# Optimization experiments

Measured on AMD Instinct MI355X. Metric: run time of the kernel, lower is better.

Reference implementation:

```python
import jax, jax.numpy as jnp
import numpy as np

N = 30000      # nodes
E = 300000     # directed edges (self loops added in conv)
G = 128        # graphs in the batch
IN = 128       # input_dim
HID = 64       # hidden per head
HEADS = 4
NC = 10        # num_classes
EPS = 1e-5
SLOPE = 0.2    # GATv2 leaky_relu negative slope


def setup_inputs() -> dict:
    key = jax.random.key(0)
    ks = jax.random.split(key, 40)
    d = {}
    d['x'] = jax.random.normal(ks[0], (N, IN), jnp.float32)
    d['edge_index'] = jax.random.randint(ks[1], (2, E), 0, N, jnp.int32)
    d['batch'] = jnp.sort(jax.random.randint(ks[2], (N,), 0, G, jnp.int32))
    in_ch = [IN, HID * HEADS, HID * HEADS, HID * HEADS]
    for i in range(4):
        oc = HID * HEADS if i < 3 else HID  # last layer concat=False -> HID
        sc = 1.0 / np.sqrt(in_ch[i])
        d[f'Wl{i}'] = jax.random.normal(ks[3 + 6 * i], (in_ch[i], HID * HEADS), jnp.float32) * sc
        d[f'Wr{i}'] = jax.random.normal(ks[4 + 6 * i], (in_ch[i], HID * HEADS), jnp.float32) * sc
        d[f'att{i}'] = jax.random.normal(ks[5 + 6 * i], (HEADS, HID), jnp.float32) * 0.1
        d[f'b{i}'] = jnp.zeros((oc,), jnp.float32)
        d[f'bng{i}'] = jnp.ones((oc,), jnp.float32)
        d[f'bnb{i}'] = jnp.zeros((oc,), jnp.float32)
    d['fc1_w'] = jax.random.normal(ks[30], (HID, HID), jnp.float32) / np.sqrt(HID)
    d['fc1_b'] = jnp.zeros((HID,), jnp.float32)
    d['fc2_w'] = jax.random.normal(ks[31], (HID, NC), jnp.float32) / np.sqrt(HID)
    d['fc2_b'] = jnp.zeros((NC,), jnp.float32)
    return d


def _gatv2_conv(h, src, dst, Wl, Wr, att, b, concat):
    # GATv2Conv: x_l = lin_l(x) for sources, x_r = lin_r(x) for targets
    xl = (h @ Wl).reshape(N, HEADS, HID)
    xr = (h @ Wr).reshape(N, HEADS, HID)
    z = jax.nn.leaky_relu(xl[src] + xr[dst], SLOPE)       # [Et, H, C]
    e = jnp.einsum('ehc,hc->eh', z, att)                   # [Et, H]
    m = jax.ops.segment_max(e, dst, num_segments=N)        # per-dst max
    p = jnp.exp(e - m[dst])
    s = jax.ops.segment_sum(p, dst, num_segments=N)
    alpha = p / s[dst]                                     # segment softmax
    msg = alpha[..., None] * xl[src]                       # [Et, H, C]
    out = jax.ops.segment_sum(msg, dst, num_segments=N)    # [N, H, C]
    out = out.reshape(N, HEADS * HID) if concat else out.mean(axis=1)
    return out + b


def _bn_train(h, g, b):
    mu = h.mean(axis=0)
    var = h.var(axis=0)  # biased, as torch BN uses for normalization
    return g * (h - mu) * jax.lax.rsqrt(var + EPS) + b


def _forward(x, edge_index, batch,
             Wl0, Wr0, att0, b0, bng0, bnb0,
             Wl1, Wr1, att1, b1, bng1, bnb1,
             Wl2, Wr2, att2, b2, bng2, bnb2,
             Wl3, Wr3, att3, b3, bng3, bnb3,
             fc1_w, fc1_b, fc2_w, fc2_b):
    loops = jnp.arange(N, dtype=edge_index.dtype)
    src = jnp.concatenate([edge_index[0], loops])  # add_self_loops=True
    dst = jnp.concatenate([edge_index[1], loops])
    layers = [(Wl0, Wr0, att0, b0, bng0, bnb0, True),
              (Wl1, Wr1, att1, b1, bng1, bnb1, True),
              (Wl2, Wr2, att2, b2, bng2, bnb2, True),
              (Wl3, Wr3, att3, b3, bng3, bnb3, False)]
    h = x
    for Wl, Wr, att, b, g, bb, concat in layers:
        h = jax.nn.elu(_bn_train(_gatv2_conv(h, src, dst, Wl, Wr, att, b, concat), g, bb))
    sums = jax.ops.segment_sum(h, batch, num_segments=G)
    cnt = jax.ops.segment_sum(jnp.ones((N,), h.dtype), batch, num_segments=G)
    pooled = sums / jnp.maximum(cnt, 1.0)[:, None]         # global_mean_pool
    o = jax.nn.relu(pooled @ fc1_w + fc1_b)
    return o @ fc2_w + fc2_b                               # dropout off (eval)


def reference(x, edge_index, batch,
              Wl0, Wr0, att0, b0, bng0, bnb0,
              Wl1, Wr1, att1, b1, bng1, bnb1,
              Wl2, Wr2, att2, b2, bng2, bnb2,
              Wl3, Wr3, att3, b3, bng3, bnb3,
              fc1_w, fc1_b, fc2_w, fc2_b):
    return _forward(x, edge_index, batch,
                    Wl0, Wr0, att0, b0, bng0, bnb0,
                    Wl1, Wr1, att1, b1, bng1, bnb1,
                    Wl2, Wr2, att2, b2, bng2, bnb2,
                    Wl3, Wr3, att3, b3, bng3, bnb3,
                    fc1_w, fc1_b, fc2_w, fc2_b)
```

## Files before the change

### kernel.cpp

```cpp
#include <hip/hip_runtime.h>
#include <hip/hip_bf16.h>
#include <math.h>

#define NN    30000
#define MPAD  30080
#define EE    300000
#define ETOT  330000
#define GG    128
#define IND   128
#define HIDD  64
#define NHEAD 4
#define CC    256
#define NCL   10
#define EPSBN 1e-5f
#define SLOPE 0.2f

typedef __attribute__((ext_vector_type(8))) __bf16 bf16x8;
typedef __attribute__((ext_vector_type(4))) float f32x4;

__device__ inline float b2f(unsigned u16) {
    union { unsigned i; float f; } c; c.i = u16 << 16; return c.f;
}
__device__ inline unsigned short f2b(float f) {
    __hip_bfloat16 b = __float2bfloat16(f);
    unsigned short u; __builtin_memcpy(&u, &b, 2); return u;
}
__device__ inline void unpack8(uint4 u, float* f) {
    f[0] = b2f(u.x & 0xffffu); f[1] = b2f(u.x >> 16);
    f[2] = b2f(u.y & 0xffffu); f[3] = b2f(u.y >> 16);
    f[4] = b2f(u.z & 0xffffu); f[5] = b2f(u.z >> 16);
    f[6] = b2f(u.w & 0xffffu); f[7] = b2f(u.w >> 16);
}

__global__ void k_deg(const int* __restrict__ ei, int* __restrict__ deg) {
    int e = blockIdx.x * blockDim.x + threadIdx.x;
    if (e >= ETOT) return;
    int d = (e < EE) ? ei[EE + e] : (e - EE);
    atomicAdd(&deg[d], 1);
}

__global__ void k_scan(const int* __restrict__ deg, int* __restrict__ rowptr,
                       int* __restrict__ cursor) {
    const int PER = 30;
    int t = threadIdx.x;
    int base = t * PER;
    int loc[PER];
    int s = 0;
    #pragma unroll
    for (int j = 0; j < PER; ++j) {
        int v = (base + j < NN) ? deg[base + j] : 0;
        loc[j] = s; s += v;
    }
    int lane = t & 63, wid = t >> 6;
    int v = s;
    #pragma unroll
    for (int d = 1; d < 64; d <<= 1) {
        int u = __shfl_up(v, d, 64);
        if (lane >= d) v += u;
    }
    __shared__ int wsum[16], woff[16];
    if (lane == 63) wsum[wid] = v;
    __syncthreads();
    if (t == 0) { int a = 0; for (int w2 = 0; w2 < 16; ++w2) { woff[w2] = a; a += wsum[w2]; } }
    __syncthreads();
    int excl = woff[wid] + (v - s);
    #pragma unroll
    for (int j = 0; j < PER; ++j) {
        int idx = base + j;
        if (idx <= NN) { int val = excl + loc[j]; rowptr[idx] = val; cursor[idx] = val; }
    }
}

__global__ void k_scatter(const int* __restrict__ ei, int* __restrict__ cursor,
                          int* __restrict__ csrc) {
    int e = blockIdx.x * blockDim.x + threadIdx.x;
    if (e >= ETOT) return;
    int s, d;
    if (e < EE) { s = ei[e]; d = ei[EE + e]; } else { s = e - EE; d = s; }
    int pos = atomicAdd(&cursor[d], 1);
    csrc[pos] = s;
}

struct WPtrs { const float* wl[4]; const float* wr[4]; };

__global__ void k_prep(WPtrs p, const float* __restrict__ x,
                       __hip_bfloat16* __restrict__ wt, __hip_bfloat16* __restrict__ hb) {
    int id = blockIdx.x * 256 + threadIdx.x;
    if (id < 65536) {
        int n = id >> 7, k = id & 127;
        float v = (n < 256) ? p.wl[0][(size_t)k * 256 + n] : p.wr[0][(size_t)k * 256 + n - 256];
        wt[id] = __float2bfloat16(v);
    } else if (id < 458752) {
        int id2 = id - 65536;
        int li = 1 + (id2 >> 17);
        int r = id2 & 131071;
        int n = r >> 8, k = r & 255;
        float v = (n < 256) ? p.wl[li][(size_t)k * 256 + n] : p.wr[li][(size_t)k * 256 + n - 256];
        wt[id] = __float2bfloat16(v);
    } else {
        int id2 = id - 458752;
        if (id2 < NN * IND) hb[id2] = __float2bfloat16(x[id2]);
    }
}

template<int K>
__global__ __launch_bounds__(256) void k_gemm_mfma(
        const __hip_bfloat16* __restrict__ A, const __hip_bfloat16* __restrict__ Wt,
        __hip_bfloat16* __restrict__ xlb, __hip_bfloat16* __restrict__ xrb) {
    __shared__ __bf16 As[128 * 40];
    __shared__ __bf16 Bs[128 * 40];
    const int t = threadIdx.x;
    const int row0 = blockIdx.x * 128;
    const int col0 = blockIdx.y * 128;
    const int wv = t >> 6, lane = t & 63;
    const int wm = (wv & 1) * 64, wn = (wv >> 1) * 64;
    const int lm = lane & 15, lq = lane >> 4;
    const int sr0 = t >> 2, scc = (t & 3) * 8;
    const int sr1 = sr0 + 64;
    uint4 va0, va1, vb0, vb1;
    va0 = *(const uint4*)&A [(size_t)(row0 + sr0) * K + scc];
    va1 = *(const uint4*)&A [(size_t)(row0 + sr1) * K + scc];
    vb0 = *(const uint4*)&Wt[(size_t)(col0 + sr0) * K + scc];
    vb1 = *(const uint4*)&Wt[(size_t)(col0 + sr1) * K + scc];
    f32x4 acc[4][4] = {};
    for (int k0 = 0; k0 < K; k0 += 32) {
        *(uint4*)&As[sr0 * 40 + scc] = va0;
        *(uint4*)&As[sr1 * 40 + scc] = va1;
        *(uint4*)&Bs[sr0 * 40 + scc] = vb0;
        *(uint4*)&Bs[sr1 * 40 + scc] = vb1;
        __syncthreads();
        if (k0 + 32 < K) {
            int kn = k0 + 32;
            va0 = *(const uint4*)&A [(size_t)(row0 + sr0) * K + kn + scc];
            va1 = *(const uint4*)&A [(size_t)(row0 + sr1) * K + kn + scc];
            vb0 = *(const uint4*)&Wt[(size_t)(col0 + sr0) * K + kn + scc];
            vb1 = *(const uint4*)&Wt[(size_t)(col0 + sr1) * K + kn + scc];
        }
        bf16x8 af[4], bfr[4];
        #pragma unroll
        for (int i = 0; i < 4; ++i) {
            af[i]  = *(bf16x8*)&As[(wm + i * 16 + lm) * 40 + lq * 8];
            bfr[i] = *(bf16x8*)&Bs[(wn + i * 16 + lm) * 40 + lq * 8];
        }
        #pragma unroll
        for (int i = 0; i < 4; ++i)
            #pragma unroll
            for (int j = 0; j < 4; ++j)
                acc[i][j] = __builtin_amdgcn_mfma_f32_16x16x32_bf16(af[i], bfr[j], acc[i][j], 0, 0, 0);
        __syncthreads();
    }
    const int crow = lq * 4;
    __hip_bfloat16* O = (blockIdx.y < 2) ? xlb : xrb;
    const int cbase = (blockIdx.y & 1) * 128 + wn;
    #pragma unroll
    for (int j = 0; j < 4; ++j) {
        int oc = cbase + j * 16 + lm;
        #pragma unroll
        for (int i = 0; i < 4; ++i) {
            int grow = row0 + wm + i * 16 + crow;
            #pragma unroll
            for (int r = 0; r < 4; ++r)
                O[(size_t)(grow + r) * CC + oc] = __float2bfloat16(acc[i][j][r]);
        }
    }
}

template<bool CONCAT>
__global__ __launch_bounds__(256) void k_gat(const __hip_bfloat16* __restrict__ xlb,
        const __hip_bfloat16* __restrict__ xrb, const int* __restrict__ rowptr,
        const int* __restrict__ csrc, const float* __restrict__ att,
        __hip_bfloat16* __restrict__ outb, float* __restrict__ outf) {
    const int wv = threadIdx.x >> 6, lane = threadIdx.x & 63;
    const int n = blockIdx.x * 4 + wv;
    if (n >= NN) return;
    const int sub = lane >> 5, l5 = lane & 31;
    const float4* att4 = (const float4*)att;
    float4 a0 = att4[l5 * 2], a1 = att4[l5 * 2 + 1];
    float aw[8] = {a0.x, a0.y, a0.z, a0.w, a1.x, a1.y, a1.z, a1.w};
    const uint4* xl4 = (const uint4*)xlb;
    const uint4* xr4 = (const uint4*)xrb;
    float xrv[8]; unpack8(xr4[(size_t)n * 32 + l5], xrv);
    const int beg = rowptr[n], end = rowptr[n + 1];
    float ssum = 0.f;
    float acc[8] = {};
    for (int i0 = beg; i0 < end; i0 += 2) {
        int i = i0 + sub;
        bool valid = i < end;
        int s = csrc[valid ? i : end - 1];
        float xlv[8]; unpack8(xl4[(size_t)s * 32 + l5], xlv);
        float tv = 0.f;
        #pragma unroll
        for (int j = 0; j < 8; ++j) {
            float v = xlv[j] + xrv[j];
            v = fmaxf(v, SLOPE * v);
            tv = fmaf(v, aw[j], tv);
        }
        tv += __shfl_xor(tv, 1);
        tv += __shfl_xor(tv, 2);
        tv += __shfl_xor(tv, 4);
        float p = valid ? __expf(tv) : 0.f;
        ssum += p;
        #pragma unroll
        for (int j = 0; j < 8; ++j) acc[j] = fmaf(p, xlv[j], acc[j]);
    }
    ssum += __shfl_xor(ssum, 32);
    #pragma unroll
    for (int j = 0; j < 8; ++j) acc[j] += __shfl_xor(acc[j], 32);
    float inv = 1.f / ssum;
    if (CONCAT) {
        if (sub == 0) {
            unsigned short r[8];
            #pragma unroll
            for (int j = 0; j < 8; ++j) r[j] = f2b(acc[j] * inv);
            uint4 o;
            o.x = r[0] | ((unsigned)r[1] << 16); o.y = r[2] | ((unsigned)r[3] << 16);
            o.z = r[4] | ((unsigned)r[5] << 16); o.w = r[6] | ((unsigned)r[7] << 16);
            ((uint4*)outb)[(size_t)n * 32 + l5] = o;
        }
    } else {
        float v[8];
        #pragma unroll
        for (int j = 0; j < 8; ++j) {
            v[j] = acc[j] * inv;
            v[j] += __shfl_xor(v[j], 8);
            v[j] += __shfl_xor(v[j], 16);
            v[j] *= 0.25f;
        }
        if (lane < 8) {
            ((float4*)outf)[(size_t)n * 16 + lane * 2]     = make_float4(v[0], v[1], v[2], v[3]);
            ((float4*)outf)[(size_t)n * 16 + lane * 2 + 1] = make_float4(v[4], v[5], v[6], v[7]);
        }
    }
}

__global__ __launch_bounds__(256) void k_bnstats256b(const __hip_bfloat16* __restrict__ in,
                                                     float* __restrict__ stats) {
    __shared__ float sh[512];
    int r0 = blockIdx.x * 128;
    int rend = min(r0 + 128, NN);
    int t = threadIdx.x;
    int half = t >> 7, tc = t & 127;
    float s0 = 0.f, s1 = 0.f, q0 = 0.f, q1 = 0.f;
    const unsigned* u32 = (const unsigned*)in;
    for (int r = r0 + half; r < rend; r += 2) {
        unsigned w = u32[(size_t)r * 128 + tc];
        float a = b2f(w & 0xffffu), b = b2f(w >> 16);
        s0 += a; q0 += a * a; s1 += b; q1 += b * b;
    }
    if (half) {
        sh[tc * 4 + 0] = s0; sh[tc * 4 + 1] = s1;
        sh[tc * 4 + 2] = q0; sh[tc * 4 + 3] = q1;
    }
    __syncthreads();
    if (!half) {
        s0 += sh[tc * 4 + 0]; s1 += sh[tc * 4 + 1];
        q0 += sh[tc * 4 + 2]; q1 += sh[tc * 4 + 3];
        atomicAdd(&stats[2 * tc], s0);       atomicAdd(&stats[2 * tc + 1], s1);
        atomicAdd(&stats[256 + 2 * tc], q0); atomicAdd(&stats[256 + 2 * tc + 1], q1);
    }
}

__global__ __launch_bounds__(256) void k_bnelu256b(const __hip_bfloat16* __restrict__ in,
        const float* __restrict__ stats, const float* __restrict__ gamma,
        const float* __restrict__ beta, __hip_bfloat16* __restrict__ outb) {
    int id = blockIdx.x * 256 + threadIdx.x;
    if (id >= NN * 32) return;
    int c0 = (id & 31) * 8;
    uint4 u = ((const uint4*)in)[id];
    float f[8]; unpack8(u, f);
    unsigned short r[8];
    #pragma unroll
    for (int j = 0; j < 8; ++j) {
        int c = c0 + j;
        float mu  = stats[c] * (1.f / NN);
        float var = stats[256 + c] * (1.f / NN) - mu * mu;
        float w = gamma[c] * rsqrtf(var + EPSBN);
        float v = w * (f[j] - mu) + beta[c];
        v = (v > 0.f) ? v : (__expf(v) - 1.f);
        r[j] = f2b(v);
    }
    uint4 o;
    o.x = r[0] | ((unsigned)r[1] << 16); o.y = r[2] | ((unsigned)r[3] << 16);
    o.z = r[4] | ((unsigned)r[5] << 16); o.w = r[6] | ((unsigned)r[7] << 16);
    ((uint4*)outb)[id] = o;
}

__global__ void k_bnstats64(const float* __restrict__ h, float* __restrict__ stats) {
    int r0 = blockIdx.x * 128;
    int rend = min(r0 + 128, NN);
    int c = threadIdx.x & 63;
    int ro = threadIdx.x >> 6;
    float s = 0.f, q = 0.f;
    for (int r = r0 + ro; r < rend; r += 4) {
        float v = h[(size_t)r * 64 + c];
        s += v; q += v * v;
    }
    atomicAdd(&stats[c], s); atomicAdd(&stats[64 + c], q);
}

__global__ void k_pool(const float* __restrict__ h, const int* __restrict__ batch,
                       const float* __restrict__ stats, const float* __restrict__ gamma,
                       const float* __restrict__ beta,
                       float* __restrict__ pooled, float* __restrict__ cnt) {
    int wv = threadIdx.x >> 6, lane = threadIdx.x & 63;
    int w = blockIdx.x * 4 + wv;
    int n0 = w * 64;
    if (n0 >= NN) return;
    int n1 = min(n0 + 64, NN);
    float mu  = stats[lane] * (1.f / NN);
    float var = stats[64 + lane] * (1.f / NN) - mu * mu;
    float sc = gamma[lane] * rsqrtf(var + EPSBN);
    float sh = beta[lane] - mu * sc;
    float sum = 0.f;
    int cur = batch[n0], c = 0;
    for (int n = n0; n < n1; ++n) {
        int g = batch[n];
        if (g != cur) {
            atomicAdd(&pooled[cur * 64 + lane], sum);
            if (lane == 0) atomicAdd(&cnt[cur], (float)c);
            sum = 0.f; c = 0; cur = g;
        }
        float v = fmaf(h[(size_t)n * 64 + lane], sc, sh);
        v = (v > 0.f) ? v : (__expf(v) - 1.f);
        sum += v;
        ++c;
    }
    atomicAdd(&pooled[cur * 64 + lane], sum);
    if (lane == 0) atomicAdd(&cnt[cur], (float)c);
}

__global__ void k_mlp(const float* __restrict__ pooled, const float* __restrict__ cnt,
        const float* __restrict__ w1, const float* __restrict__ b1,
        const float* __restrict__ w2, const float* __restrict__ b2,
        float* __restrict__ out) {
    __shared__ float p[64], o[64];
    int g = blockIdx.x, t = threadIdx.x;
    float c = fmaxf(cnt[g], 1.f);
    p[t] = pooled[g * 64 + t] / c;
    __syncthreads();
    float s = b1[t];
    for (int k = 0; k < 64; ++k) s += p[k] * w1[k * 64 + t];
    o[t] = fmaxf(s, 0.f);
    __syncthreads();
    if (t < NCL) {
        float s2 = b2[t];
        for (int k = 0; k < 64; ++k) s2 += o[k] * w2[k * NCL + t];
        out[g * NCL + t] = s2;
    }
}

extern "C" void kernel_launch(void* const* d_in, const int* in_sizes, int n_in,
                              void* d_out, int out_size, void* d_ws, size_t ws_size,
                              hipStream_t stream) {
    const float* x     = (const float*)d_in[0];
    const int*   ei    = (const int*)d_in[1];
    const int*   batch = (const int*)d_in[2];
    WPtrs wp;
    const float *attp[4], *bng[4], *bnb[4];
    for (int i = 0; i < 4; ++i) {
        wp.wl[i] = (const float*)d_in[3 + 6 * i];
        wp.wr[i] = (const float*)d_in[4 + 6 * i];
        attp[i]  = (const float*)d_in[5 + 6 * i];
        bng[i]   = (const float*)d_in[7 + 6 * i];
        bnb[i]   = (const float*)d_in[8 + 6 * i];
    }
    const float* fc1w = (const float*)d_in[27];
    const float* fc1b = (const float*)d_in[28];
    const float* fc2w = (const float*)d_in[29];
    const float* fc2b = (const float*)d_in[30];
    float* out = (float*)d_out;

    char* w = (char*)d_ws;
    __hip_bfloat16* xlb  = (__hip_bfloat16*)w; w += (size_t)MPAD * CC * 2;
    __hip_bfloat16* xrb  = (__hip_bfloat16*)w; w += (size_t)MPAD * CC * 2;
    __hip_bfloat16* bufB = (__hip_bfloat16*)w; w += (size_t)MPAD * CC * 2;
    __hip_bfloat16* hb   = (__hip_bfloat16*)w; w += (size_t)MPAD * CC * 2;
    __hip_bfloat16* wt   = (__hip_bfloat16*)w; w += (size_t)458752 * 2;
    float* bufF   = (float*)w; w += (size_t)NN * HIDD * 4;
    int*   rowptr = (int*)w;   w += (size_t)(NN + 1) * 4;
    int*   cursor = (int*)w;   w += (size_t)(NN + 1) * 4;
    int*   csrc   = (int*)w;   w += (size_t)ETOT * 4;
    char* zbase = w;
    int*   deg       = (int*)w;   w += (size_t)NN * 4;
    float* stats_all = (float*)w; w += (size_t)4 * 512 * 4;
    float* pooled    = (float*)w; w += (size_t)GG * HIDD * 4;
    float* cnt       = (float*)w; w += (size_t)GG * 4;
    size_t zbytes = (size_t)(w - zbase);

    __hip_bfloat16* Wt[4];
    Wt[0] = wt;
    Wt[1] = wt + 65536;
    Wt[2] = wt + 65536 + 131072;
    Wt[3] = wt + 65536 + 262144;

    hipMemsetAsync(zbase, 0, zbytes, stream);
    k_deg<<<(ETOT + 255) / 256, 256, 0, stream>>>(ei, deg);
    k_scan<<<1, 1024, 0, stream>>>(deg, rowptr, cursor);
    k_scatter<<<(ETOT + 255) / 256, 256, 0, stream>>>(ei, cursor, csrc);
    k_prep<<<(458752 + NN * IND + 255) / 256, 256, 0, stream>>>(wp, x, wt, hb);

    for (int L = 0; L < 4; ++L) {
        float* stats = stats_all + 512 * L;
        dim3 gg(MPAD / 128, 4);
        if (L == 0) k_gemm_mfma<IND><<<gg, 256, 0, stream>>>(hb, Wt[0], xlb, xrb);
        else        k_gemm_mfma<CC><<<gg, 256, 0, stream>>>(hb, Wt[L], xlb, xrb);
        if (L < 3) {
            k_gat<true><<<NN / 4, 256, 0, stream>>>(xlb, xrb, rowptr, csrc, attp[L], bufB, nullptr);
            k_bnstats256b<<<(NN + 127) / 128, 256, 0, stream>>>(bufB, stats);
            k_bnelu256b<<<(NN * 32 + 255) / 256, 256, 0, stream>>>(bufB, stats, bng[L], bnb[L], hb);
        } else {
            k_gat<false><<<NN / 4, 256, 0, stream>>>(xlb, xrb, rowptr, csrc, attp[3], nullptr, bufF);
            k_bnstats64<<<(NN + 127) / 128, 256, 0, stream>>>(bufF, stats);
        }
    }
    k_pool<<<((NN + 63) / 64 + 3) / 4, 256, 0, stream>>>(bufF, batch, stats_all + 512 * 3,
                                                         bng[3], bnb[3], pooled, cnt);
    k_mlp<<<GG, 64, 0, stream>>>(pooled, cnt, fc1w, fc1b, fc2w, fc2b, out);
}
```

Measured before the change: 599.0 us.

## Merge setup kernels, widen GEMM K-tile, and use packed float2 math in GAT

Fuses the degree-count and weight/input bf16 conversion kernels into one launch, removing a kernel launch. The MFMA GEMM now stages 64-wide K slices per barrier instead of 32, halving the number of sync iterations at the cost of more LDS and registers. The GAT aggregation kernel uses two-wide float vector arithmetic so the compiler can emit packed FP32 instructions for the leaky-relu, attention dot product and accumulation.

```diff
diff --git a/kernel.cpp b/kernel.cpp
--- a/kernel.cpp
+++ b/kernel.cpp
@@ -17,6 +17,7 @@
 
 typedef __attribute__((ext_vector_type(8))) __bf16 bf16x8;
 typedef __attribute__((ext_vector_type(4))) float f32x4;
+typedef __attribute__((ext_vector_type(2))) float f32x2;
 
 __device__ inline float b2f(unsigned u16) {
     union { unsigned i; float f; } c; c.i = u16 << 16; return c.f;
@@ -24,6 +25,12 @@
 __device__ inline unsigned short f2b(float f) {
     __hip_bfloat16 b = __float2bfloat16(f);
     unsigned short u; __builtin_memcpy(&u, &b, 2); return u;
+}
+__device__ inline f32x2 upk(unsigned u) {
+    union { unsigned i; float f; } lo, hi;
+    lo.i = u << 16;
+    hi.i = u & 0xffff0000u;
+    f32x2 r; r.x = lo.f; r.y = hi.f; return r;
 }
 __device__ inline void unpack8(uint4 u, float* f) {
     f[0] = b2f(u.x & 0xffffu); f[1] = b2f(u.x >> 16);
@@ -32,11 +39,33 @@
     f[6] = b2f(u.w & 0xffffu); f[7] = b2f(u.w >> 16);
 }
 
-__global__ void k_deg(const int* __restrict__ ei, int* __restrict__ deg) {
-    int e = blockIdx.x * blockDim.x + threadIdx.x;
-    if (e >= ETOT) return;
-    int d = (e < EE) ? ei[EE + e] : (e - EE);
-    atomicAdd(&deg[d], 1);
+struct WPtrs { const float* wl[4]; const float* wr[4]; };
+
+__global__ void k_setup(const int* __restrict__ ei, int* __restrict__ deg,
+                        WPtrs p, const float* __restrict__ x,
+                        __hip_bfloat16* __restrict__ wt, __hip_bfloat16* __restrict__ hb) {
+    int id = blockIdx.x * 256 + threadIdx.x;
+    if (id < ETOT) {
+        int d = (id < EE) ? ei[EE + id] : (id - EE);
+        atomicAdd(&deg[d], 1);
+        return;
+    }
+    int id1 = id - ETOT;
+    if (id1 < 65536) {
+        int n = id1 >> 7, k = id1 & 127;
+        float v = (n < 256) ? p.wl[0][(size_t)k * 256 + n] : p.wr[0][(size_t)k * 256 + n - 256];
+        wt[id1] = __float2bfloat16(v);
+    } else if (id1 < 458752) {
+        int id2 = id1 - 65536;
+        int li = 1 + (id2 >> 17);
+        int r = id2 & 131071;
+        int n = r >> 8, k = r & 255;
+        float v = (n < 256) ? p.wl[li][(size_t)k * 256 + n] : p.wr[li][(size_t)k * 256 + n - 256];
+        wt[id1] = __float2bfloat16(v);
+    } else {
+        int id2 = id1 - 458752;
+        if (id2 < NN * IND) hb[id2] = __float2bfloat16(x[id2]);
+    }
 }
 
 __global__ void k_scan(const int* __restrict__ deg, int* __restrict__ rowptr,
@@ -81,72 +110,56 @@
     csrc[pos] = s;
 }
 
-struct WPtrs { const float* wl[4]; const float* wr[4]; };
-
-__global__ void k_prep(WPtrs p, const float* __restrict__ x,
-                       __hip_bfloat16* __restrict__ wt, __hip_bfloat16* __restrict__ hb) {
-    int id = blockIdx.x * 256 + threadIdx.x;
-    if (id < 65536) {
-        int n = id >> 7, k = id & 127;
-        float v = (n < 256) ? p.wl[0][(size_t)k * 256 + n] : p.wr[0][(size_t)k * 256 + n - 256];
-        wt[id] = __float2bfloat16(v);
-    } else if (id < 458752) {
-        int id2 = id - 65536;
-        int li = 1 + (id2 >> 17);
-        int r = id2 & 131071;
-        int n = r >> 8, k = r & 255;
-        float v = (n < 256) ? p.wl[li][(size_t)k * 256 + n] : p.wr[li][(size_t)k * 256 + n - 256];
-        wt[id] = __float2bfloat16(v);
-    } else {
-        int id2 = id - 458752;
-        if (id2 < NN * IND) hb[id2] = __float2bfloat16(x[id2]);
-    }
-}
-
 template<int K>
 __global__ __launch_bounds__(256) void k_gemm_mfma(
         const __hip_bfloat16* __restrict__ A, const __hip_bfloat16* __restrict__ Wt,
         __hip_bfloat16* __restrict__ xlb, __hip_bfloat16* __restrict__ xrb) {
-    __shared__ __bf16 As[128 * 40];
-    __shared__ __bf16 Bs[128 * 40];
+    __shared__ __bf16 As[128 * 72];
+    __shared__ __bf16 Bs[128 * 72];
     const int t = threadIdx.x;
     const int row0 = blockIdx.x * 128;
     const int col0 = blockIdx.y * 128;
     const int wv = t >> 6, lane = t & 63;
     const int wm = (wv & 1) * 64, wn = (wv >> 1) * 64;
     const int lm = lane & 15, lq = lane >> 4;
-    const int sr0 = t >> 2, scc = (t & 3) * 8;
-    const int sr1 = sr0 + 64;
-    uint4 va0, va1, vb0, vb1;
-    va0 = *(const uint4*)&A [(size_t)(row0 + sr0) * K + scc];
-    va1 = *(const uint4*)&A [(size_t)(row0 + sr1) * K + scc];
-    vb0 = *(const uint4*)&Wt[(size_t)(col0 + sr0) * K + scc];
-    vb1 = *(const uint4*)&Wt[(size_t)(col0 + sr1) * K + scc];
+    const int sr = t >> 1;
+    const int sh = (t & 1) * 32;
+    uint4 va[4], vb[4];
+    #pragma unroll
+    for (int i = 0; i < 4; ++i) {
+        va[i] = *(const uint4*)&A [(size_t)(row0 + sr) * K + sh + i * 8];
+        vb[i] = *(const uint4*)&Wt[(size_t)(col0 + sr) * K + sh + i * 8];
+    }
     f32x4 acc[4][4] = {};
-    for (int k0 = 0; k0 < K; k0 += 32) {
-        *(uint4*)&As[sr0 * 40 + scc] = va0;
-        *(uint4*)&As[sr1 * 40 + scc] = va1;
-        *(uint4*)&Bs[sr0 * 40 + scc] = vb0;
-        *(uint4*)&Bs[sr1 * 40 + scc] = vb1;
+    for (int k0 = 0; k0 < K; k0 += 64) {
+        #pragma unroll
+        for (int i = 0; i < 4; ++i) {
+            *(uint4*)&As[sr * 72 + sh + i * 8] = va[i];
+            *(uint4*)&Bs[sr * 72 + sh + i * 8] = vb[i];
+        }
         __syncthreads();
-        if (k0 + 32 < K) {
-            int kn = k0 + 32;
-            va0 = *(const uint4*)&A [(size_t)(row0 + sr0) * K + kn + scc];
-            va1 = *(const uint4*)&A [(size_t)(row0 + sr1) * K + kn + scc];
-            vb0 = *(const uint4*)&Wt[(size_t)(col0 + sr0) * K + kn + scc];
-            vb1 = *(const uint4*)&Wt[(size_t)(col0 + sr1) * K + kn + scc];
-        }
-        bf16x8 af[4], bfr[4];
-        #pragma unroll
-        for (int i = 0; i < 4; ++i) {
-            af[i]  = *(bf16x8*)&As[(wm + i * 16 + lm) * 40 + lq * 8];
-            bfr[i] = *(bf16x8*)&Bs[(wn + i * 16 + lm) * 40 + lq * 8];
-        }
-        #pragma unroll
-        for (int i = 0; i < 4; ++i)
+        if (k0 + 64 < K) {
+            int kn = k0 + 64;
             #pragma unroll
-            for (int j = 0; j < 4; ++j)
-                acc[i][j] = __builtin_amdgcn_mfma_f32_16x16x32_bf16(af[i], bfr[j], acc[i][j], 0, 0, 0);
+            for (int i = 0; i < 4; ++i) {
+                va[i] = *(const uint4*)&A [(size_t)(row0 + sr) * K + kn + sh + i * 8];
+                vb[i] = *(const uint4*)&Wt[(size_t)(col0 + sr) * K + kn + sh + i * 8];
+            }
+        }
+        #pragma unroll
+        for (int kk = 0; kk < 2; ++kk) {
+            bf16x8 af[4], bfr[4];
+            #pragma unroll
+            for (int i = 0; i < 4; ++i) {
+                af[i]  = *(bf16x8*)&As[(wm + i * 16 + lm) * 72 + kk * 32 + lq * 8];
+                bfr[i] = *(bf16x8*)&Bs[(wn + i * 16 + lm) * 72 + kk * 32 + lq * 8];
+            }
+            #pragma unroll
+            for (int i = 0; i < 4; ++i)
+                #pragma unroll
+                for (int j = 0; j < 4; ++j)
+                    acc[i][j] = __builtin_amdgcn_mfma_f32_16x16x32_bf16(af[i], bfr[j], acc[i][j], 0, 0, 0);
+        }
         __syncthreads();
     }
     const int crow = lq * 4;
@@ -176,42 +189,52 @@
     const int sub = lane >> 5, l5 = lane & 31;
     const float4* att4 = (const float4*)att;
     float4 a0 = att4[l5 * 2], a1 = att4[l5 * 2 + 1];
-    float aw[8] = {a0.x, a0.y, a0.z, a0.w, a1.x, a1.y, a1.z, a1.w};
+    f32x2 aw[4];
+    aw[0].x = a0.x; aw[0].y = a0.y; aw[1].x = a0.z; aw[1].y = a0.w;
+    aw[2].x = a1.x; aw[2].y = a1.y; aw[3].x = a1.z; aw[3].y = a1.w;
     const uint4* xl4 = (const uint4*)xlb;
     const uint4* xr4 = (const uint4*)xrb;
-    float xrv[8]; unpack8(xr4[(size_t)n * 32 + l5], xrv);
+    uint4 xru = xr4[(size_t)n * 32 + l5];
+    f32x2 xr2[4] = {upk(xru.x), upk(xru.y), upk(xru.z), upk(xru.w)};
     const int beg = rowptr[n], end = rowptr[n + 1];
     float ssum = 0.f;
-    float acc[8] = {};
+    f32x2 acc[4] = {};
+    const f32x2 slope2 = {SLOPE, SLOPE};
     for (int i0 = beg; i0 < end; i0 += 2) {
         int i = i0 + sub;
         bool valid = i < end;
         int s = csrc[valid ? i : end - 1];
-        float xlv[8]; unpack8(xl4[(size_t)s * 32 + l5], xlv);
-        float tv = 0.f;
-        #pragma unroll
-        for (int j = 0; j < 8; ++j) {
-            float v = xlv[j] + xrv[j];
-            v = fmaxf(v, SLOPE * v);
-            tv = fmaf(v, aw[j], tv);
-        }
+        uint4 xu = xl4[(size_t)s * 32 + l5];
+        f32x2 xl2[4] = {upk(xu.x), upk(xu.y), upk(xu.z), upk(xu.w)};
+        f32x2 tv2 = {0.f, 0.f};
+        #pragma unroll
+        for (int j = 0; j < 4; ++j) {
+            f32x2 v = xl2[j] + xr2[j];
+            v = __builtin_elementwise_max(v, v * slope2);
+            tv2 = __builtin_elementwise_fma(v, aw[j], tv2);
+        }
+        float tv = tv2.x + tv2.y;
         tv += __shfl_xor(tv, 1);
         tv += __shfl_xor(tv, 2);
         tv += __shfl_xor(tv, 4);
         float p = valid ? __expf(tv) : 0.f;
         ssum += p;
-        #pragma unroll
-        for (int j = 0; j < 8; ++j) acc[j] = fmaf(p, xlv[j], acc[j]);
+        f32x2 p2 = {p, p};
+        #pragma unroll
+        for (int j = 0; j < 4; ++j)
+            acc[j] = __builtin_elementwise_fma(p2, xl2[j], acc[j]);
     }
     ssum += __shfl_xor(ssum, 32);
-    #pragma unroll
-    for (int j = 0; j < 8; ++j) acc[j] += __shfl_xor(acc[j], 32);
+    float a[8] = {acc[0].x, acc[0].y, acc[1].x, acc[1].y,
+                  acc[2].x, acc[2].y, acc[3].x, acc[3].y};
+    #pragma unroll
+    for (int j = 0; j < 8; ++j) a[j] += __shfl_xor(a[j], 32);
     float inv = 1.f / ssum;
     if (CONCAT) {
         if (sub == 0) {
             unsigned short r[8];
             #pragma unroll
-            for (int j = 0; j < 8; ++j) r[j] = f2b(acc[j] * inv);
+            for (int j = 0; j < 8; ++j) r[j] = f2b(a[j] * inv);
             uint4 o;
             o.x = r[0] | ((unsigned)r[1] << 16); o.y = r[2] | ((unsigned)r[3] << 16);
             o.z = r[4] | ((unsigned)r[5] << 16); o.w = r[6] | ((unsigned)r[7] << 16);
@@ -221,7 +244,7 @@
         float v[8];
         #pragma unroll
         for (int j = 0; j < 8; ++j) {
-            v[j] = acc[j] * inv;
+            v[j] = a[j] * inv;
             v[j] += __shfl_xor(v[j], 8);
             v[j] += __shfl_xor(v[j], 16);
             v[j] *= 0.25f;
@@ -394,10 +417,9 @@
     Wt[3] = wt + 65536 + 262144;
 
     hipMemsetAsync(zbase, 0, zbytes, stream);
-    k_deg<<<(ETOT + 255) / 256, 256, 0, stream>>>(ei, deg);
+    k_setup<<<(ETOT + 458752 + NN * IND + 255) / 256, 256, 0, stream>>>(ei, deg, wp, x, wt, hb);
     k_scan<<<1, 1024, 0, stream>>>(deg, rowptr, cursor);
     k_scatter<<<(ETOT + 255) / 256, 256, 0, stream>>>(ei, cursor, csrc);
-    k_prep<<<(458752 + NN * IND + 255) / 256, 256, 0, stream>>>(wp, x, wt, hb);
 
     for (int L = 0; L < 4; ++L) {
         float* stats = stats_all + 512 * L;
```

After: 705.7 us. 1.18x slower.
